# Optimization experiments

Hardware: AMD Instinct MI355X
Metric: run time of the kernel (lower is better)

Reference implementation:

```python
import jax, jax.numpy as jnp
import numpy as np

N_LAYERS = 4
N_WIRES = 10


def _apply_1q(state, U, wire, n):
    # state: [B, 2^n] complex64; U: [2,2] or [B,2,2]
    B = state.shape[0]
    a, b = 2 ** wire, 2 ** (n - wire - 1)
    s = state.reshape(B, a, 2, b)
    if U.ndim == 2:
        s = jnp.einsum('ij,bxjy->bxiy', U, s)
    else:
        s = jnp.einsum('bij,bxjy->bxiy', U, s)
    return s.reshape(B, -1)


def _apply_cnot(state, c, t, n):
    # CNOT with control c, target t (wire 0 = most significant bit, PennyLane convention)
    B = state.shape[0]
    q1, q2 = min(c, t), max(c, t)
    d1, d2, d3 = 2 ** q1, 2 ** (q2 - q1 - 1), 2 ** (n - q2 - 1)
    s = state.reshape(B, d1, 2, d2, 2, d3)
    if c < t:
        # control on axis 2, flip (X) target axis 4 where control bit == 1
        s = jnp.concatenate([s[:, :, 0:1], jnp.flip(s[:, :, 1:2], axis=4)], axis=2)
    else:
        # control on axis 4, flip target axis 2 where control bit == 1
        s = jnp.concatenate([s[:, :, :, :, 0:1], jnp.flip(s[:, :, :, :, 1:2], axis=2)], axis=4)
    return s.reshape(B, -1)


def _ry_mat(theta):
    # theta: [B] -> [B,2,2] complex64
    c, s = jnp.cos(theta / 2), jnp.sin(theta / 2)
    return jnp.stack([jnp.stack([c, -s], -1), jnp.stack([s, c], -1)], -2).astype(jnp.complex64)


def _rot_mat(phi, theta, omega):
    # qml.Rot(phi, theta, omega) = RZ(omega) @ RY(theta) @ RZ(phi)
    e = lambda a: jnp.exp(1j * a.astype(jnp.complex64))
    c = jnp.cos(theta / 2).astype(jnp.complex64)
    s = jnp.sin(theta / 2).astype(jnp.complex64)
    m00 = e(-0.5 * (phi + omega)) * c
    m01 = -e(0.5 * (phi - omega)) * s
    m10 = e(-0.5 * (phi - omega)) * s
    m11 = e(0.5 * (phi + omega)) * c
    return jnp.stack([jnp.stack([m00, m01]), jnp.stack([m10, m11])])


def setup_inputs() -> dict:
    key = jax.random.key(0)
    kx, kw = jax.random.split(key)
    X = jax.random.uniform(kx, (16384, N_WIRES), dtype=jnp.float32)
    # weightsStrongly = pi * U(0,1) of shape (n_layers, n_wires, 3)
    weights = np.pi * jax.random.uniform(kw, (N_LAYERS, N_WIRES, 3), dtype=jnp.float32)
    bias = jnp.zeros((1,), dtype=jnp.float32)
    return {"X": X, "weights": weights, "bias": bias}


def reference(X, weights, bias):
    B, n = X.shape
    L = weights.shape[0]
    # |0...0> batched statevector
    state = jnp.zeros((B, 2 ** n), dtype=jnp.complex64).at[:, 0].set(1.0)
    # angle encoding, gates='Y': RY(x_i * pi/2) on wire i (per-sample angle)
    for w in range(n):
        state = _apply_1q(state, _ry_mat(X[:, w] * (np.pi / 2)), w, n)
    # StronglyEntanglingLayers: Rot on each wire, then ring of CNOTs with range r_l
    for l in range(L):
        for w in range(n):
            U = _rot_mat(weights[l, w, 0], weights[l, w, 1], weights[l, w, 2])
            state = _apply_1q(state, U, w, n)
        r = l % (n - 1) + 1
        for w in range(n):
            state = _apply_cnot(state, w, (w + r) % n, n)
    # numClasses=2 -> single measurement: expval(PauliZ(wire n-1)) (last wire = LSB)
    probs = (state.real ** 2 + state.imag ** 2).reshape(B, 2 ** (n - 1), 2)
    z = jnp.sum(probs[..., 0] - probs[..., 1], axis=-1)  # [B]
    return z[:, None] + bias[None, :]  # [B, 1]
```

## Files before the change

### kernel.cpp

```cpp
#include <hip/hip_runtime.h>
#include <cstdint>
#include <utility>

#define NW 10
#define NL 4


typedef float v2 __attribute__((ext_vector_type(2)));

struct Cols10 { unsigned c[10]; };
struct Rows10 { unsigned r[10]; };

constexpr Cols10 TMAT = {{
    0x001, 0x002, 0x004, 0x008,
    0x070, 0x080, 0x100, 0x130, 0x210, 0x200
}};

constexpr unsigned tmap(unsigned m) {
    unsigned r = 0;
    for (int b = 0; b < 10; ++b) if ((m >> b) & 1u) r ^= TMAT.c[b];
    return r;
}

constexpr Rows10 invertT() {
    unsigned a[10] = {}, inv[10] = {};
    for (int i = 0; i < 10; ++i) {
        for (int j = 0; j < 10; ++j) a[i] |= ((TMAT.c[j] >> i) & 1u) << j;
        inv[i] = 1u << i;
    }
    for (int col = 0; col < 10; ++col) {
        int piv = -1;
        for (int r2 = col; r2 < 10; ++r2) if ((a[r2] >> col) & 1u) { piv = r2; break; }
        unsigned ta = a[piv]; a[piv] = a[col]; a[col] = ta;
        unsigned ti = inv[piv]; inv[piv] = inv[col]; inv[col] = ti;
        for (int r2 = 0; r2 < 10; ++r2)
            if (r2 != col && ((a[r2] >> col) & 1u)) { a[r2] ^= a[col]; inv[r2] ^= inv[col]; }
    }
    Rows10 R{};
    for (int i = 0; i < 10; ++i) R.r[i] = inv[i];
    return R;
}
constexpr Rows10 RROW = invertT();

constexpr unsigned rmap(unsigned rowmask) {
    unsigned r = 0;
    for (int b = 0; b < 10; ++b) if ((rowmask >> b) & 1u) r ^= RROW.r[b];
    return r;
}

static_assert(RROW.r[0] == 1 && RROW.r[1] == 2 && RROW.r[2] == 4 && RROW.r[3] == 8, "slot rows");
static_assert((RROW.r[4] & 15) == 0 && (RROW.r[5] & 15) == 0 && (RROW.r[6] & 15) == 0 &&
              (RROW.r[7] & 15) == 0 && (RROW.r[8] & 15) == 0 && (RROW.r[9] & 15) == 0, "lane rows");

struct Plan {
    int n;
    uint16_t pmask[40];
    uint16_t rmask[40];
    uint8_t  lw[40];
    uint16_t measmask;
};

constexpr bool keep_rot(int l, int w) {
    if (l <= 1) return true;
    if (l == 2) return w != 7;
    return w == 1 || w == 5 || w == 9;
}

constexpr Plan make_plan() {
    Plan P{};
    unsigned row[10], cI[10];
    for (int b = 0; b < 10; ++b) { row[b] = 1u << b; cI[b] = 1u << b; }
    P.n = 0;
    for (int l = 0; l < NL; ++l) {
        for (int w = 0; w < NW; ++w) {
            if (l > 0 && keep_rot(l, w)) {
                const int b = 9 - w;
                P.pmask[P.n] = (uint16_t)tmap(cI[b]);
                P.rmask[P.n] = (uint16_t)rmap(row[b]);
                P.lw[P.n]    = (uint8_t)(l * NW + w);
                P.n++;
            }
        }
        const int r = l % (NW - 1) + 1;
        for (int w = 0; w < NW; ++w) {
            const int cb = 9 - w, tb = 9 - ((w + r) % NW);
            row[tb] ^= row[cb];
            cI[cb]  ^= cI[tb];
        }
    }
    P.measmask = (uint16_t)rmap(row[0]);
    return P;
}

constexpr Plan PL = make_plan();
constexpr int NROT = 22;
static_assert(PL.n == NROT, "plan size mismatch");

constexpr int LSEL[6] = {
    (int)(RROW.r[9] >> 4), (int)(RROW.r[8] >> 4), (int)(RROW.r[7] >> 4),
    (int)(RROW.r[6] >> 4), (int)(RROW.r[5] >> 4), (int)(RROW.r[4] >> 4)
};

template<int MASK>
__device__ __forceinline__ float swz(float v, int lane) {
    if constexpr (MASK == 1) {
        return __int_as_float(__builtin_amdgcn_mov_dpp(__float_as_int(v), 0xB1, 0xF, 0xF, true));
    } else if constexpr (MASK == 2) {
        return __int_as_float(__builtin_amdgcn_mov_dpp(__float_as_int(v), 0x4E, 0xF, 0xF, true));
    } else if constexpr (MASK == 3) {
        return __int_as_float(__builtin_amdgcn_mov_dpp(__float_as_int(v), 0x1B, 0xF, 0xF, true));
    } else if constexpr (MASK == 7) {
        return __int_as_float(__builtin_amdgcn_mov_dpp(__float_as_int(v), 0x141, 0xF, 0xF, true));
    } else if constexpr (MASK == 15) {
        return __int_as_float(__builtin_amdgcn_mov_dpp(__float_as_int(v), 0x140, 0xF, 0xF, true));
    } else if constexpr (MASK < 32) {
        return __int_as_float(__builtin_amdgcn_ds_swizzle(
            __float_as_int(v), (MASK << 10) | 0x1F));
    } else {
        return __int_as_float(__builtin_amdgcn_ds_bpermute(
            (lane << 2) ^ (MASK << 2), __float_as_int(v)));
    }
}

template<int MASK>
__device__ __forceinline__ v2 swz2(v2 v, int lane) {
    v2 r;
    r.x = swz<MASK>(v.x, lane);
    r.y = swz<MASK>(v.y, lane);
    return r;
}

__device__ __forceinline__ v2 mkv2(float a, float b) { v2 r; r.x = a; r.y = b; return r; }

__device__ __forceinline__ void cmul2(v2 ar, v2 ai, v2 br, v2 bi, v2& cr, v2& ci) {
    cr = ar * br - ai * bi;
    ci = ar * bi + ai * br;
}

__device__ __forceinline__ void upd(v2& xr, v2& xi, v2 pr, v2 pi,
                                    float cmr, float coi, float bmi, float bor,
                                    bool S) {
    const float emi = S ? -bmi : bmi;
    const float eor = S ? -bor : bor;
    const v2 nr = cmr * xr - emi * xi + eor * pr - coi * pi;
    const v2 ni = cmr * xi + emi * xr + eor * pi + coi * pr;
    xr = nr; xi = ni;
}

template<int G>
__device__ __forceinline__ void apply_rot(v2 (&sr)[16], v2 (&si)[16],
                                          const float4* __restrict__ rotm,
                                          int lane) {
    constexpr unsigned pm = PL.pmask[G], rm = PL.rmask[G];
    constexpr int pLoc = pm & 15, pLane = (int)(pm >> 4);
    constexpr int rLoc = rm & 15, rLane = (int)(rm >> 4);
    const float4 m = rotm[PL.lw[G]];
    const bool rl = (__popc(lane & rLane) & 1) != 0;
    const float cmr = m.x, coi = m.w;
    const float bmi = rl ? -m.y : m.y;
    const float bor = rl ? -m.z : m.z;

    if constexpr (pLane == 0) {
#pragma unroll
        for (int j = 0; j < 16; ++j) {
            const int k = j ^ pLoc;
            if (j < k) {
                const v2 ajr = sr[j], aji = si[j];
                const v2 akr = sr[k], aki = si[k];
                upd(sr[j], si[j], akr, aki, cmr, coi, bmi, bor,
                    (__builtin_popcount(j & rLoc) & 1) != 0);
                upd(sr[k], si[k], ajr, aji, cmr, coi, bmi, bor,
                    (__builtin_popcount(k & rLoc) & 1) != 0);
            }
        }
    } else if constexpr (pLoc == 0) {
#pragma unroll
        for (int j = 0; j < 16; ++j) {
            const v2 pr = swz2<pLane>(sr[j], lane);
            const v2 pi = swz2<pLane>(si[j], lane);
            upd(sr[j], si[j], pr, pi, cmr, coi, bmi, bor,
                (__builtin_popcount(j & rLoc) & 1) != 0);
        }
    } else {
#pragma unroll
        for (int j = 0; j < 16; ++j) {
            const int k = j ^ pLoc;
            if (j < k) {
                const v2 pjr = swz2<pLane>(sr[k], lane);
                const v2 pji = swz2<pLane>(si[k], lane);
                const v2 pkr = swz2<pLane>(sr[j], lane);
                const v2 pki = swz2<pLane>(si[j], lane);
                upd(sr[j], si[j], pjr, pji, cmr, coi, bmi, bor,
                    (__builtin_popcount(j & rLoc) & 1) != 0);
                upd(sr[k], si[k], pkr, pki, cmr, coi, bmi, bor,
                    (__builtin_popcount(k & rLoc) & 1) != 0);
            }
        }
    }
}

template<int... Gs>
__device__ __forceinline__ void apply_all(v2 (&sr)[16], v2 (&si)[16],
                                          const float4* __restrict__ rotm,
                                          int lane,
                                          std::integer_sequence<int, Gs...>) {
    (apply_rot<Gs>(sr, si, rotm, lane), ...);
}

__global__ __launch_bounds__(256, 2) void vqc_kernel(const float* __restrict__ X,
                                                     const float* __restrict__ W,
                                                     const float* __restrict__ bias,
                                                     float* __restrict__ out,
                                                     int n_pairs) {
    __shared__ float4 rotm[NL * NW];
    const int t = threadIdx.x;

    if (t < NL * NW) {
        const float phi = W[t * 3 + 0], th = W[t * 3 + 1], om = W[t * 3 + 2];
        float sh, ch; sincosf(0.5f * th, &sh, &ch);
        float s0, c0; sincosf(-0.5f * (phi + om), &s0, &c0);
        float s1, c1; sincosf( 0.5f * (phi - om), &s1, &c1);
        rotm[t] = make_float4(c0 * ch, s0 * ch, -c1 * sh, -s1 * sh);
    }
    __syncthreads();

    const int wave = (blockIdx.x * blockDim.x + t) >> 6;
    const int lane = t & 63;
    if (wave >= n_pairs) return;

    const float* xp = X + (size_t)(2 * wave) * NW;

    v2 hr, hi;
#pragma unroll
    for (int w = 0; w < 6; ++w) {
        float s0, c0, s1, c1;
        __sincosf(xp[w]      * 0.78539816339744831f, &s0, &c0);
        __sincosf(xp[w + NW] * 0.78539816339744831f, &s1, &c1);
        const v2 s = mkv2(s0, s1), c = mkv2(c0, c1);
        const float4 m = rotm[w];
        const v2 a0r = m.x * c + m.z * s;
        const v2 a0i = m.y * c + m.w * s;
        const v2 a1r = m.x * s - m.z * c;
        const v2 a1i = m.w * c - m.y * s;
        const bool b = (__popc(lane & LSEL[w]) & 1) != 0;
        const v2 br = b ? a1r : a0r;
        const v2 bi = b ? a1i : a0i;
        if (w == 0) { hr = br; hi = bi; }
        else {
            v2 nr, ni; cmul2(hr, hi, br, bi, nr, ni);
            hr = nr; hi = ni;
        }
    }
    v2 t0r[4], t0i[4], t1r[4], t1i[4];
#pragma unroll
    for (int w = 6; w < 10; ++w) {
        float s0, c0, s1, c1;
        __sincosf(xp[w]      * 0.78539816339744831f, &s0, &c0);
        __sincosf(xp[w + NW] * 0.78539816339744831f, &s1, &c1);
        const v2 s = mkv2(s0, s1), c = mkv2(c0, c1);
        const float4 m = rotm[w];
        t0r[w - 6] = m.x * c + m.z * s;
        t0i[w - 6] = m.y * c + m.w * s;
        t1r[w - 6] = m.x * s - m.z * c;
        t1i[w - 6] = m.w * c - m.y * s;
    }
    v2 Ar[4], Ai[4], Br[4], Bi[4];
#pragma unroll
    for (int u = 0; u < 4; ++u) {
        const int hb = (u >> 1) & 1, lb = u & 1;
        cmul2(hb ? t1r[0] : t0r[0], hb ? t1i[0] : t0i[0],
              lb ? t1r[1] : t0r[1], lb ? t1i[1] : t0i[1], Ar[u], Ai[u]);
        cmul2(hb ? t1r[2] : t0r[2], hb ? t1i[2] : t0i[2],
              lb ? t1r[3] : t0r[3], lb ? t1i[3] : t0i[3], Br[u], Bi[u]);
    }
    v2 HAr[4], HAi[4];
#pragma unroll
    for (int u = 0; u < 4; ++u) cmul2(hr, hi, Ar[u], Ai[u], HAr[u], HAi[u]);

    v2 sr[16], si[16];
#pragma unroll
    for (int j = 0; j < 16; ++j) {
        cmul2(HAr[j >> 2], HAi[j >> 2], Br[j & 3], Bi[j & 3], sr[j], si[j]);
    }

    apply_all(sr, si, rotm, lane, std::make_integer_sequence<int, NROT>{});

    constexpr unsigned mm = PL.measmask;
    constexpr int mLoc = mm & 15, mLane = (int)(mm >> 4);
    v2 acc = mkv2(0.0f, 0.0f);
#pragma unroll
    for (int j = 0; j < 16; ++j) {
        const v2 p = sr[j] * sr[j] + si[j] * si[j];
        if (__builtin_popcount(j & mLoc) & 1) acc -= p; else acc += p;
    }
    if (__popc(lane & mLane) & 1) acc = -acc;
    acc += swz2<1>(acc, lane);
    acc += swz2<2>(acc, lane);
    acc += swz2<4>(acc, lane);
    acc += swz2<8>(acc, lane);
    acc += swz2<16>(acc, lane);
    acc += swz2<32>(acc, lane);
    if (lane == 0) {
        const float b0 = bias[0];
        out[2 * wave]     = acc.x + b0;
        out[2 * wave + 1] = acc.y + b0;
    }
}

extern "C" void kernel_launch(void* const* d_in, const int* in_sizes, int n_in,
                              void* d_out, int out_size, void* d_ws, size_t ws_size,
                              hipStream_t stream) {
    const float* X    = (const float*)d_in[0];
    const float* W    = (const float*)d_in[1];
    const float* bias = (const float*)d_in[2];
    float* out = (float*)d_out;
    const int n_samples = in_sizes[0] / NW;
    const int n_pairs = n_samples / 2;
    const int threads = 256;
    const int blocks = (n_pairs * 64 + threads - 1) / threads;
    hipLaunchKernelGGL(vqc_kernel, dim3(blocks), dim3(threads), 0, stream,
                       X, W, bias, out, n_pairs);
}
```

Before: 126.8 us.

## Switch from two-samples-per-wave SIMD pairs to one sample per wave with packed complex

Each wave now handles one sample instead of two. The complex amplitudes are packed as (re, im) float2 pairs, so the rotation update runs as packed math using lane swaps of the complex components. This halves the register state per thread and doubles the wave count, and launch_bounds min-blocks is dropped. The trade-off is twice as many cross-lane swizzle reductions and swizzle ops per sample, and packed math now covers only one sample's re/im rather than two samples.

```diff
diff --git a/kernel.cpp b/kernel.cpp
--- a/kernel.cpp
+++ b/kernel.cpp
@@ -131,24 +131,16 @@
 }
 
 __device__ __forceinline__ v2 mkv2(float a, float b) { v2 r; r.x = a; r.y = b; return r; }
-
-__device__ __forceinline__ void cmul2(v2 ar, v2 ai, v2 br, v2 bi, v2& cr, v2& ci) {
-    cr = ar * br - ai * bi;
-    ci = ar * bi + ai * br;
-}
-
-__device__ __forceinline__ void upd(v2& xr, v2& xi, v2 pr, v2 pi,
-                                    float cmr, float coi, float bmi, float bor,
-                                    bool S) {
-    const float emi = S ? -bmi : bmi;
-    const float eor = S ? -bor : bor;
-    const v2 nr = cmr * xr - emi * xi + eor * pr - coi * pi;
-    const v2 ni = cmr * xi + emi * xr + eor * pi + coi * pr;
-    xr = nr; xi = ni;
+__device__ __forceinline__ v2 cswap(v2 v) { return __builtin_shufflevector(v, v, 1, 0); }
+
+__device__ __forceinline__ v2 rot_core(v2 z, v2 p, v2 cm2, v2 e1, v2 eo2, v2 c1, bool S) {
+    const v2 ea = S ? -e1 : e1;
+    const v2 eb = S ? -eo2 : eo2;
+    return cm2 * z + ea * cswap(z) + eb * p + c1 * cswap(p);
 }
 
 template<int G>
-__device__ __forceinline__ void apply_rot(v2 (&sr)[16], v2 (&si)[16],
+__device__ __forceinline__ void apply_rot(v2 (&S)[16],
                                           const float4* __restrict__ rotm,
                                           int lane) {
     constexpr unsigned pm = PL.pmask[G], rm = PL.rmask[G];
@@ -156,62 +148,67 @@
     constexpr int rLoc = rm & 15, rLane = (int)(rm >> 4);
     const float4 m = rotm[PL.lw[G]];
     const bool rl = (__popc(lane & rLane) & 1) != 0;
-    const float cmr = m.x, coi = m.w;
     const float bmi = rl ? -m.y : m.y;
     const float bor = rl ? -m.z : m.z;
+    const v2 cm2 = mkv2(m.x, m.x);
+    const v2 e1  = mkv2(-bmi, bmi);
+    const v2 eo2 = mkv2(bor, bor);
+    const v2 c1  = mkv2(-m.w, m.w);
 
     if constexpr (pLane == 0) {
 #pragma unroll
         for (int j = 0; j < 16; ++j) {
             const int k = j ^ pLoc;
             if (j < k) {
-                const v2 ajr = sr[j], aji = si[j];
-                const v2 akr = sr[k], aki = si[k];
-                upd(sr[j], si[j], akr, aki, cmr, coi, bmi, bor,
-                    (__builtin_popcount(j & rLoc) & 1) != 0);
-                upd(sr[k], si[k], ajr, aji, cmr, coi, bmi, bor,
-                    (__builtin_popcount(k & rLoc) & 1) != 0);
+                const v2 zj = S[j], zk = S[k];
+                S[j] = rot_core(zj, zk, cm2, e1, eo2, c1,
+                                (__builtin_popcount(j & rLoc) & 1) != 0);
+                S[k] = rot_core(zk, zj, cm2, e1, eo2, c1,
+                                (__builtin_popcount(k & rLoc) & 1) != 0);
             }
         }
     } else if constexpr (pLoc == 0) {
 #pragma unroll
         for (int j = 0; j < 16; ++j) {
-            const v2 pr = swz2<pLane>(sr[j], lane);
-            const v2 pi = swz2<pLane>(si[j], lane);
-            upd(sr[j], si[j], pr, pi, cmr, coi, bmi, bor,
-                (__builtin_popcount(j & rLoc) & 1) != 0);
+            const v2 p = swz2<pLane>(S[j], lane);
+            S[j] = rot_core(S[j], p, cm2, e1, eo2, c1,
+                            (__builtin_popcount(j & rLoc) & 1) != 0);
         }
     } else {
 #pragma unroll
         for (int j = 0; j < 16; ++j) {
             const int k = j ^ pLoc;
             if (j < k) {
-                const v2 pjr = swz2<pLane>(sr[k], lane);
-                const v2 pji = swz2<pLane>(si[k], lane);
-                const v2 pkr = swz2<pLane>(sr[j], lane);
-                const v2 pki = swz2<pLane>(si[j], lane);
-                upd(sr[j], si[j], pjr, pji, cmr, coi, bmi, bor,
-                    (__builtin_popcount(j & rLoc) & 1) != 0);
-                upd(sr[k], si[k], pkr, pki, cmr, coi, bmi, bor,
-                    (__builtin_popcount(k & rLoc) & 1) != 0);
+                const v2 pj = swz2<pLane>(S[k], lane);
+                const v2 pk = swz2<pLane>(S[j], lane);
+                S[j] = rot_core(S[j], pj, cm2, e1, eo2, c1,
+                                (__builtin_popcount(j & rLoc) & 1) != 0);
+                S[k] = rot_core(S[k], pk, cm2, e1, eo2, c1,
+                                (__builtin_popcount(k & rLoc) & 1) != 0);
             }
         }
     }
 }
 
 template<int... Gs>
-__device__ __forceinline__ void apply_all(v2 (&sr)[16], v2 (&si)[16],
+__device__ __forceinline__ void apply_all(v2 (&S)[16],
                                           const float4* __restrict__ rotm,
                                           int lane,
                                           std::integer_sequence<int, Gs...>) {
-    (apply_rot<Gs>(sr, si, rotm, lane), ...);
-}
-
-__global__ __launch_bounds__(256, 2) void vqc_kernel(const float* __restrict__ X,
-                                                     const float* __restrict__ W,
-                                                     const float* __restrict__ bias,
-                                                     float* __restrict__ out,
-                                                     int n_pairs) {
+    (apply_rot<Gs>(S, rotm, lane), ...);
+}
+
+__device__ __forceinline__ void cmul(float ar, float ai, float br, float bi,
+                                     float& cr, float& ci) {
+    cr = ar * br - ai * bi;
+    ci = ar * bi + ai * br;
+}
+
+__global__ __launch_bounds__(256) void vqc_kernel(const float* __restrict__ X,
+                                                  const float* __restrict__ W,
+                                                  const float* __restrict__ bias,
+                                                  float* __restrict__ out,
+                                                  int n_samples) {
     __shared__ float4 rotm[NL * NW];
     const int t = threadIdx.x;
 
@@ -226,85 +223,74 @@
 
     const int wave = (blockIdx.x * blockDim.x + t) >> 6;
     const int lane = t & 63;
-    if (wave >= n_pairs) return;
-
-    const float* xp = X + (size_t)(2 * wave) * NW;
-
-    v2 hr, hi;
-#pragma unroll
-    for (int w = 0; w < 6; ++w) {
-        float s0, c0, s1, c1;
-        __sincosf(xp[w]      * 0.78539816339744831f, &s0, &c0);
-        __sincosf(xp[w + NW] * 0.78539816339744831f, &s1, &c1);
-        const v2 s = mkv2(s0, s1), c = mkv2(c0, c1);
+    if (wave >= n_samples) return;
+
+    const float* xp = X + (size_t)wave * NW;
+    float v0r[NW], v0i[NW], v1r[NW], v1i[NW];
+#pragma unroll
+    for (int w = 0; w < NW; ++w) {
+        float s, c;
+        __sincosf(xp[w] * 0.78539816339744831f, &s, &c);
         const float4 m = rotm[w];
-        const v2 a0r = m.x * c + m.z * s;
-        const v2 a0i = m.y * c + m.w * s;
-        const v2 a1r = m.x * s - m.z * c;
-        const v2 a1i = m.w * c - m.y * s;
-        const bool b = (__popc(lane & LSEL[w]) & 1) != 0;
-        const v2 br = b ? a1r : a0r;
-        const v2 bi = b ? a1i : a0i;
-        if (w == 0) { hr = br; hi = bi; }
-        else {
-            v2 nr, ni; cmul2(hr, hi, br, bi, nr, ni);
+        v0r[w] =  m.x * c + m.z * s;
+        v0i[w] =  m.y * c + m.w * s;
+        v1r[w] = -m.z * c + m.x * s;
+        v1i[w] =  m.w * c - m.y * s;
+    }
+    float hr, hi;
+    {
+        const bool b0 = (__popc(lane & LSEL[0]) & 1) != 0;
+        hr = b0 ? v1r[0] : v0r[0];
+        hi = b0 ? v1i[0] : v0i[0];
+#pragma unroll
+        for (int w = 1; w < 6; ++w) {
+            const bool b = (__popc(lane & LSEL[w]) & 1) != 0;
+            const float br = b ? v1r[w] : v0r[w];
+            const float bi = b ? v1i[w] : v0i[w];
+            float nr, ni; cmul(hr, hi, br, bi, nr, ni);
             hr = nr; hi = ni;
         }
     }
-    v2 t0r[4], t0i[4], t1r[4], t1i[4];
-#pragma unroll
-    for (int w = 6; w < 10; ++w) {
-        float s0, c0, s1, c1;
-        __sincosf(xp[w]      * 0.78539816339744831f, &s0, &c0);
-        __sincosf(xp[w + NW] * 0.78539816339744831f, &s1, &c1);
-        const v2 s = mkv2(s0, s1), c = mkv2(c0, c1);
-        const float4 m = rotm[w];
-        t0r[w - 6] = m.x * c + m.z * s;
-        t0i[w - 6] = m.y * c + m.w * s;
-        t1r[w - 6] = m.x * s - m.z * c;
-        t1i[w - 6] = m.w * c - m.y * s;
-    }
-    v2 Ar[4], Ai[4], Br[4], Bi[4];
+    float Ar[4], Ai[4], Br[4], Bi[4];
 #pragma unroll
     for (int u = 0; u < 4; ++u) {
         const int hb = (u >> 1) & 1, lb = u & 1;
-        cmul2(hb ? t1r[0] : t0r[0], hb ? t1i[0] : t0i[0],
-              lb ? t1r[1] : t0r[1], lb ? t1i[1] : t0i[1], Ar[u], Ai[u]);
-        cmul2(hb ? t1r[2] : t0r[2], hb ? t1i[2] : t0i[2],
-              lb ? t1r[3] : t0r[3], lb ? t1i[3] : t0i[3], Br[u], Bi[u]);
-    }
-    v2 HAr[4], HAi[4];
-#pragma unroll
-    for (int u = 0; u < 4; ++u) cmul2(hr, hi, Ar[u], Ai[u], HAr[u], HAi[u]);
-
-    v2 sr[16], si[16];
+        cmul(hb ? v1r[6] : v0r[6], hb ? v1i[6] : v0i[6],
+             lb ? v1r[7] : v0r[7], lb ? v1i[7] : v0i[7], Ar[u], Ai[u]);
+        cmul(hb ? v1r[8] : v0r[8], hb ? v1i[8] : v0i[8],
+             lb ? v1r[9] : v0r[9], lb ? v1i[9] : v0i[9], Br[u], Bi[u]);
+    }
+    float HAr[4], HAi[4];
+#pragma unroll
+    for (int u = 0; u < 4; ++u) cmul(hr, hi, Ar[u], Ai[u], HAr[u], HAi[u]);
+
+    v2 S[16];
 #pragma unroll
     for (int j = 0; j < 16; ++j) {
-        cmul2(HAr[j >> 2], HAi[j >> 2], Br[j & 3], Bi[j & 3], sr[j], si[j]);
-    }
-
-    apply_all(sr, si, rotm, lane, std::make_integer_sequence<int, NROT>{});
+        float r0, i0;
+        cmul(HAr[j >> 2], HAi[j >> 2], Br[j & 3], Bi[j & 3], r0, i0);
+        S[j] = mkv2(r0, i0);
+    }
+
+    apply_all(S, rotm, lane, std::make_integer_sequence<int, NROT>{});
 
     constexpr unsigned mm = PL.measmask;
     constexpr int mLoc = mm & 15, mLane = (int)(mm >> 4);
-    v2 acc = mkv2(0.0f, 0.0f);
+    float acc = 0.0f;
 #pragma unroll
     for (int j = 0; j < 16; ++j) {
-        const v2 p = sr[j] * sr[j] + si[j] * si[j];
-        if (__builtin_popcount(j & mLoc) & 1) acc -= p; else acc += p;
+        const v2 sq = S[j] * S[j];
+        const float p = sq.x + sq.y;
+        acc += ((__builtin_popcount(j & mLoc) & 1) ? -p : p);
     }
     if (__popc(lane & mLane) & 1) acc = -acc;
-    acc += swz2<1>(acc, lane);
-    acc += swz2<2>(acc, lane);
-    acc += swz2<4>(acc, lane);
-    acc += swz2<8>(acc, lane);
-    acc += swz2<16>(acc, lane);
-    acc += swz2<32>(acc, lane);
-    if (lane == 0) {
-        const float b0 = bias[0];
-        out[2 * wave]     = acc.x + b0;
-        out[2 * wave + 1] = acc.y + b0;
-    }
+    acc += swz<1>(acc, lane);
+    acc += swz<2>(acc, lane);
+    acc += swz<4>(acc, lane);
+    acc += swz<8>(acc, lane);
+    acc += swz<16>(acc, lane);
+    acc += swz<32>(acc, lane);
+    if (lane == 0) out[wave] = acc + bias[0];
 }
 
 extern "C" void kernel_launch(void* const* d_in, const int* in_sizes, int n_in,
@@ -315,9 +301,8 @@
     const float* bias = (const float*)d_in[2];
     float* out = (float*)d_out;
     const int n_samples = in_sizes[0] / NW;
-    const int n_pairs = n_samples / 2;
     const int threads = 256;
-    const int blocks = (n_pairs * 64 + threads - 1) / threads;
+    const int blocks = (n_samples * 64 + threads - 1) / threads;
     hipLaunchKernelGGL(vqc_kernel, dim3(blocks), dim3(threads), 0, stream,
-                       X, W, bias, out, n_pairs);
-}
+                       X, W, bias, out, n_samples);
+}
```

After: 132.7 us. +4.6%, slower.
